# Optimization experiments

Measured on AMD Instinct MI355X. Metric: run time of the kernel, lower is better.

Reference implementation:

```python
import jax, jax.numpy as jnp
import numpy as np

H = 8          # nhead
EPS_Z = 1e-6   # linear-attention normalizer eps
LN_EPS = 1e-5  # torch LayerNorm default


def _ln(x, g, b):
    m = x.mean(-1, keepdims=True)
    v = ((x - m) ** 2).mean(-1, keepdims=True)
    return (x - m) * jax.lax.rsqrt(v + LN_EPS) * g + b


def setup_inputs() -> dict:
    key = jax.random.key(0)
    ks = jax.random.split(key, 8)
    B, S, E, F = 4, 8192, 512, 2048
    s = 0.02
    return {
        "src": jax.random.normal(ks[0], (B, S, E), jnp.float32),
        "Wq": jax.random.normal(ks[1], (E, E), jnp.float32) * s,
        "bq": jnp.zeros((E,), jnp.float32),
        "Wk": jax.random.normal(ks[2], (E, E), jnp.float32) * s,
        "bk": jnp.zeros((E,), jnp.float32),
        "Wv": jax.random.normal(ks[3], (E, E), jnp.float32) * s,
        "bv": jnp.zeros((E,), jnp.float32),
        "Wo": jax.random.normal(ks[4], (E, E), jnp.float32) * s,
        "bo": jnp.zeros((E,), jnp.float32),
        "W1": jax.random.normal(ks[5], (E, F), jnp.float32) * s,
        "b1": jnp.zeros((F,), jnp.float32),
        "W2": jax.random.normal(ks[6], (F, E), jnp.float32) * s,
        "b2": jnp.zeros((E,), jnp.float32),
        "g1": jnp.ones((E,), jnp.float32),
        "be1": jnp.zeros((E,), jnp.float32),
        "g2": jnp.ones((E,), jnp.float32),
        "be2": jnp.zeros((E,), jnp.float32),
    }


def reference(src, Wq, bq, Wk, bk, Wv, bv, Wo, bo, W1, b1, W2, b2, g1, be1, g2, be2):
    B, S, E = src.shape
    Dh = E // H

    def heads(x):  # [B,S,E] -> [B,H,S,Dh]
        return x.reshape(B, S, H, Dh).transpose(0, 2, 1, 3)

    q = heads(src @ Wq + bq)
    k = heads(src @ Wk + bk)
    v = heads(src @ Wv + bv)

    qm = jax.nn.elu(q) + 1.0  # feature map: ELU+1
    km = jax.nn.elu(k) + 1.0

    kv = jnp.einsum("bhsd,bhse->bhde", km, v)          # [B,H,Dh,Dh]
    ksum = km.sum(axis=2)                               # [B,H,Dh]
    z = 1.0 / (jnp.einsum("bhsd,bhd->bhs", qm, ksum) + EPS_Z)
    attn = jnp.einsum("bhsd,bhde->bhse", qm, kv) * z[..., None]

    attn = attn.transpose(0, 2, 1, 3).reshape(B, S, E) @ Wo + bo
    x = _ln(src + attn, g1, be1)
    ff = jax.nn.relu(x @ W1 + b1) @ W2 + b2
    return _ln(x + ff, g2, be2)
```

## Files before the change

kernel.cpp:

```cpp
#include <hip/hip_runtime.h>
#include <hip/hip_bf16.h>

typedef __attribute__((ext_vector_type(8))) short bf16x8;
typedef __attribute__((ext_vector_type(4))) float f32x4;

__device__ inline ushort f2bf(float f) {
    uint u = __float_as_uint(f);
    u += 0x7fff + ((u >> 16) & 1);
    return (ushort)(u >> 16);
}
__device__ inline float bf2f(ushort h) {
    return __uint_as_float(((uint)h) << 16);
}

__device__ inline void gload16(const void* g, void* lds) {
    __builtin_amdgcn_global_load_lds(
        (const __attribute__((address_space(1))) void*)g,
        (__attribute__((address_space(3))) void*)lds, 16, 0, 0);
}

__global__ void conv_bf16(const float* __restrict__ in, ushort* __restrict__ out, int n4) {
    int i = blockIdx.x * 256 + threadIdx.x;
    if (i >= n4) return;
    float4 a = ((const float4*)in)[i];
    ushort4 o;
    o.x = f2bf(a.x); o.y = f2bf(a.y); o.z = f2bf(a.z); o.w = f2bf(a.w);
    ((ushort4*)out)[i] = o;
}

__global__ void wconv_t(const float* __restrict__ in, ushort* __restrict__ out, int K, int N) {
    __shared__ float tile[32][33];
    int kb = blockIdx.y * 32, nb = blockIdx.x * 32;
    int tx = threadIdx.x & 31, ty = threadIdx.x >> 5;
#pragma unroll
    for (int i = 0; i < 4; i++)
        tile[ty + i * 8][tx] = in[(size_t)(kb + ty + i * 8) * N + nb + tx];
    __syncthreads();
#pragma unroll
    for (int i = 0; i < 4; i++) {
        int n = nb + ty + i * 8, k = kb + tx;
        out[(size_t)n * K + k] = f2bf(tile[tx][ty + i * 8]);
    }
}

__global__ void biascat(const float* __restrict__ a, const float* __restrict__ b,
                        const float* __restrict__ c, float* __restrict__ o) {
    int i = blockIdx.x * 256 + threadIdx.x;
    if (i < 512) o[i] = a[i];
    else if (i < 1024) o[i] = b[i - 512];
    else if (i < 1536) o[i] = c[i - 1024];
}

template <int EPI>
__global__ __launch_bounds__(512, 2) void gemm256(
    const ushort* __restrict__ A, const ushort* __restrict__ Bt,
    const float* __restrict__ bias, const ushort* __restrict__ res16,
    ushort* __restrict__ out16, int M, int N, int K, int nbx) {
    extern __shared__ char smem[];
    const int t = threadIdx.x;
    const int w = t >> 6, l = t & 63;
    const int wr = w >> 2, wc = w & 3;
    const int nwg = gridDim.x;
    const int cpx = nwg >> 3;
    const int swz = (blockIdx.x & 7) * cpx + (blockIdx.x >> 3);
    const int bx = swz % nbx, by = swz / nbx;

    const int sc = (t & 3) ^ ((t >> 3) & 3);
    const ushort* gA0 = A + (size_t)(by * 256 + (t >> 2)) * K + sc * 8;
    const ushort* gA1 = gA0 + (size_t)128 * K;
    const ushort* gB0 = Bt + (size_t)(bx * 256 + (t >> 2)) * K + sc * 8;
    const ushort* gB1 = gB0 + (size_t)128 * K;

#define STAGE_H0(kt)                                          \
    {                                                         \
        char* Lb = smem + ((kt) & 3) * 32768 + (w << 10);     \
        const int ko_ = (kt) * 32;                            \
        gload16(gA0 + ko_, Lb);                               \
        gload16(gB0 + ko_, Lb + 16384);                       \
    }
#define STAGE_H1(kt)                                          \
    {                                                         \
        char* Lb = smem + ((kt) & 3) * 32768 + (w << 10);     \
        const int ko_ = (kt) * 32;                            \
        gload16(gA1 + ko_, Lb + 8192);                        \
        gload16(gB1 + ko_, Lb + 24576);                       \
    }

    f32x4 acc[8][4] = {};
    const int Kt = K >> 5;

    const int R0a = wr * 128 + (l & 15);
    const int offA = R0a * 64 + (((l >> 4) ^ ((R0a >> 1) & 3)) << 4);
    const int R0b = wc * 64 + (l & 15);
    const int offB = 16384 + R0b * 64 + (((l >> 4) ^ ((R0b >> 1) & 3)) << 4);

    STAGE_H0(0); STAGE_H1(0);
    STAGE_H0(1); STAGE_H1(1);
    STAGE_H0(2); STAGE_H1(2);

#pragma unroll 1
    for (int kt = 0; kt < Kt; ++kt) {
        const int rem = Kt - 1 - kt;
        if (rem >= 2)      asm volatile("s_waitcnt vmcnt(8)" ::: "memory");
        else if (rem == 1) asm volatile("s_waitcnt vmcnt(4)" ::: "memory");
        else               asm volatile("s_waitcnt vmcnt(0)" ::: "memory");
        __builtin_amdgcn_s_barrier();
        __builtin_amdgcn_sched_barrier(0);

        const char* bufp = smem + (kt & 3) * 32768;
        bf16x8 a[8], b[4];
        b[0] = *(const bf16x8*)(bufp + offB);
        b[1] = *(const bf16x8*)(bufp + offB + 1024);
        b[2] = *(const bf16x8*)(bufp + offB + 2048);
        b[3] = *(const bf16x8*)(bufp + offB + 3072);
        a[0] = *(const bf16x8*)(bufp + offA);
        a[1] = *(const bf16x8*)(bufp + offA + 1024);
        a[2] = *(const bf16x8*)(bufp + offA + 2048);
        a[3] = *(const bf16x8*)(bufp + offA + 3072);
        if (kt + 3 < Kt) STAGE_H0(kt + 3);
        __builtin_amdgcn_sched_barrier(0);
        __builtin_amdgcn_s_barrier();
        asm volatile("s_waitcnt lgkmcnt(0)" ::: "memory");
        __builtin_amdgcn_sched_barrier(0);
        __builtin_amdgcn_s_setprio(1);
#pragma unroll
        for (int m = 0; m < 4; m++)
#pragma unroll
            for (int n = 0; n < 4; n++)
                acc[m][n] = __builtin_amdgcn_mfma_f32_16x16x32_bf16(a[m], b[n], acc[m][n], 0, 0, 0);
        __builtin_amdgcn_s_setprio(0);
        __builtin_amdgcn_sched_barrier(0);
        a[4] = *(const bf16x8*)(bufp + offA + 4096);
        a[5] = *(const bf16x8*)(bufp + offA + 5120);
        a[6] = *(const bf16x8*)(bufp + offA + 6144);
        a[7] = *(const bf16x8*)(bufp + offA + 7168);
        if (kt + 3 < Kt) STAGE_H1(kt + 3);
        __builtin_amdgcn_sched_barrier(0);
        __builtin_amdgcn_s_barrier();
        asm volatile("s_waitcnt lgkmcnt(0)" ::: "memory");
        __builtin_amdgcn_sched_barrier(0);
        __builtin_amdgcn_s_setprio(1);
#pragma unroll
        for (int m = 4; m < 8; m++)
#pragma unroll
            for (int n = 0; n < 4; n++)
                acc[m][n] = __builtin_amdgcn_mfma_f32_16x16x32_bf16(a[m], b[n], acc[m][n], 0, 0, 0);
        __builtin_amdgcn_s_setprio(0);
        __builtin_amdgcn_sched_barrier(0);
    }
#undef STAGE_H0
#undef STAGE_H1

    const int row0 = by * 256 + wr * 128 + ((l >> 4) << 2);
    const int col0 = bx * 256 + wc * 64 + (l & 15);
    const int seg = bx >> 1;
    const size_t segoff = (size_t)seg * M * 512;
    const int c511 = col0 & 511;
    float bv[4];
#pragma unroll
    for (int n = 0; n < 4; n++) bv[n] = bias[col0 + n * 16];
#pragma unroll
    for (int m = 0; m < 8; m++) {
#pragma unroll
        for (int r = 0; r < 4; r++) {
            const int row = row0 + m * 16 + r;
            const size_t base = (size_t)row * N + col0;
#pragma unroll
            for (int n = 0; n < 4; n++) {
                float vv = acc[m][n][r] + bv[n];
                if constexpr (EPI == 2) {
                    vv = vv > 0.f ? vv : 0.f;
                    out16[base + n * 16] = f2bf(vv);
                } else if constexpr (EPI == 3) {
                    vv += bf2f(res16[base + n * 16]);
                    out16[base + n * 16] = f2bf(vv);
                } else if constexpr (EPI == 4) {
                    if (seg < 2) vv = vv > 0.f ? vv + 1.f : __expf(vv);
                    out16[segoff + (size_t)row * 512 + c511 + n * 16] = f2bf(vv);
                } else {
                    out16[base + n * 16] = f2bf(vv);
                }
            }
        }
    }
}

__global__ __launch_bounds__(256) void kv_partial(
    const ushort* __restrict__ km, const ushort* __restrict__ v,
    float* __restrict__ kvp, float* __restrict__ ksump, int S) {
    __shared__ ushort kms[32 * 64];
    __shared__ ushort vs[32 * 64];
    const int t = threadIdx.x;
    const int bh = blockIdx.y, b = bh >> 3, h = bh & 7;
    const int d0 = (t >> 4) * 4, e0 = (t & 15) * 4;
    float acc[4][4] = {};
    float ks = 0.f;
    const int s_base = blockIdx.x * 512;
    const int r = t >> 3, c8 = (t & 7) * 8;
    for (int s0 = 0; s0 < 512; s0 += 32) {
        size_t grow = ((size_t)b * S + s_base + s0 + r) * 512 + h * 64 + c8;
        *(uint4*)&kms[r * 64 + c8] = *(const uint4*)&km[grow];
        *(uint4*)&vs[r * 64 + c8] = *(const uint4*)&v[grow];
        __syncthreads();
#pragma unroll 4
        for (int s = 0; s < 32; ++s) {
            ushort4 ka = *(const ushort4*)&kms[s * 64 + d0];
            ushort4 vb = *(const ushort4*)&vs[s * 64 + e0];
            float a0 = bf2f(ka.x), a1 = bf2f(ka.y), a2 = bf2f(ka.z), a3 = bf2f(ka.w);
            float b0 = bf2f(vb.x), b1 = bf2f(vb.y), b2 = bf2f(vb.z), b3 = bf2f(vb.w);
            acc[0][0] += a0 * b0; acc[0][1] += a0 * b1; acc[0][2] += a0 * b2; acc[0][3] += a0 * b3;
            acc[1][0] += a1 * b0; acc[1][1] += a1 * b1; acc[1][2] += a1 * b2; acc[1][3] += a1 * b3;
            acc[2][0] += a2 * b0; acc[2][1] += a2 * b1; acc[2][2] += a2 * b2; acc[2][3] += a2 * b3;
            acc[3][0] += a3 * b0; acc[3][1] += a3 * b1; acc[3][2] += a3 * b2; acc[3][3] += a3 * b3;
            if (t < 64) ks += bf2f(kms[s * 64 + t]);
        }
        __syncthreads();
    }
    float* dst = kvp + ((size_t)bh * 16 + blockIdx.x) * 4096;
#pragma unroll
    for (int i = 0; i < 4; i++)
#pragma unroll
        for (int j = 0; j < 4; j++)
            dst[(d0 + i) * 64 + e0 + j] = acc[i][j];
    if (t < 64) ksump[((size_t)bh * 16 + blockIdx.x) * 64 + t] = ks;
}

__global__ void kv_reduce(const float* __restrict__ kvp, const float* __restrict__ ksump,
                          ushort* __restrict__ kvt, float* __restrict__ ksum) {
    int i = blockIdx.x * 256 + threadIdx.x;
    if (i < 32 * 4096) {
        int bh = i >> 12, de = i & 4095;
        int d = de >> 6, e = de & 63;
        float s = 0.f;
#pragma unroll
        for (int c = 0; c < 16; ++c) s += kvp[((size_t)bh * 16 + c) * 4096 + de];
        kvt[(size_t)bh * 4096 + e * 64 + d] = f2bf(s);
    } else {
        int j = i - 32 * 4096;
        if (j < 32 * 64) {
            int bh = j >> 6, d = j & 63;
            float s = 0.f;
#pragma unroll
            for (int c = 0; c < 16; ++c) s += ksump[((size_t)bh * 16 + c) * 64 + d];
            ksum[j] = s;
        }
    }
}

__global__ __launch_bounds__(256) void attn_mfma(
    const ushort* __restrict__ qm, const ushort* __restrict__ kvt,
    const float* __restrict__ ksum, ushort* __restrict__ attnE, int S) {
    __shared__ ushort As[128 * 128];
    __shared__ ushort Bs[128 * 64];
    __shared__ float zbuf[128][2];
    __shared__ float ks2[128];
    const int t = threadIdx.x, w = t >> 6, l = t & 63;
    const int cx = blockIdx.x, by = blockIdx.y;
    const int b = (by * 128) / S;
    const int h0 = cx * 2;
    const size_t arow0 = (size_t)(by * 128) * 512 + cx * 128;

#pragma unroll
    for (int rd = 0; rd < 8; ++rd) {
        const ushort* g = qm + arow0 + (size_t)(rd * 16 + w * 4 + (l >> 4)) * 512 + (l & 15) * 8;
        gload16(g, (char*)As + rd * 4096 + w * 1024);
    }
    const ushort* kvbase = kvt + (size_t)(b * 8 + h0) * 4096;
#pragma unroll
    for (int rd = 0; rd < 4; ++rd) {
        const ushort* g = kvbase + (rd * 32 + w * 8 + (l >> 3)) * 64 + (l & 7) * 8;
        gload16(g, (char*)Bs + rd * 4096 + w * 1024);
    }
    if (t < 128) ks2[t] = ksum[(b * 8 + h0) * 64 + t];
    __syncthreads();

    {
        const int r = t >> 1, hh = t & 1;
        float den = 0.f;
#pragma unroll
        for (int d0 = 0; d0 < 64; d0 += 8) {
            bf16x8 qv = *(const bf16x8*)&As[r * 128 + hh * 64 + d0];
#pragma unroll
            for (int j = 0; j < 8; j++) den += bf2f((ushort)qv[j]) * ks2[hh * 64 + d0 + j];
        }
        zbuf[r][hh] = 1.0f / (den + 1e-6f);
    }

    const int wr = w >> 1, wc = w & 1;
    const int ar = wr * 64 + (l & 15);
    const int br = wc * 64 + (l & 15);
    const int ko = (l >> 4) * 8;
    f32x4 acc[4][4] = {};
#pragma unroll
    for (int ks_ = 0; ks_ < 2; ++ks_) {
        bf16x8 a[4], bb[4];
#pragma unroll
        for (int m = 0; m < 4; m++)
            a[m] = *(const bf16x8*)&As[(ar + m * 16) * 128 + wc * 64 + ks_ * 32 + ko];
#pragma unroll
        for (int n = 0; n < 4; n++)
            bb[n] = *(const bf16x8*)&Bs[(br + n * 16) * 64 + ks_ * 32 + ko];
#pragma unroll
        for (int m = 0; m < 4; m++)
#pragma unroll
            for (int n = 0; n < 4; n++)
                acc[m][n] = __builtin_amdgcn_mfma_f32_16x16x32_bf16(a[m], bb[n], acc[m][n], 0, 0, 0);
    }
    __syncthreads();

    const int row0l = wr * 64 + ((l >> 4) << 2);
    ushort* outbase = attnE + (size_t)(by * 128) * 512 + cx * 128;
#pragma unroll
    for (int n = 0; n < 4; n++) {
#pragma unroll
        for (int m = 0; m < 4; m++) {
#pragma unroll
            for (int r = 0; r < 4; r++) {
                int rl = row0l + m * 16 + r;
                float z = zbuf[rl][wc];
                outbase[(size_t)rl * 512 + wc * 64 + n * 16 + (l & 15)] = f2bf(acc[m][n][r] * z);
            }
        }
    }
}

template <int OUT32>
__global__ __launch_bounds__(256) void ln_bf16(
    const ushort* __restrict__ in, const float* __restrict__ g, const float* __restrict__ be,
    void* __restrict__ outp, int Mrows) {
    const int w = threadIdx.x >> 6, l = threadIdx.x & 63;
    const int row = blockIdx.x * 4 + w;
    if (row >= Mrows) return;
    const ushort* rp = in + (size_t)row * 512;
    uint4 u = *(const uint4*)&rp[l * 8];
    float x[8];
    x[0] = bf2f((ushort)(u.x & 0xffff)); x[1] = bf2f((ushort)(u.x >> 16));
    x[2] = bf2f((ushort)(u.y & 0xffff)); x[3] = bf2f((ushort)(u.y >> 16));
    x[4] = bf2f((ushort)(u.z & 0xffff)); x[5] = bf2f((ushort)(u.z >> 16));
    x[6] = bf2f((ushort)(u.w & 0xffff)); x[7] = bf2f((ushort)(u.w >> 16));
    float s = 0.f, ss = 0.f;
#pragma unroll
    for (int j = 0; j < 8; j++) { s += x[j]; ss += x[j] * x[j]; }
#pragma unroll
    for (int o = 1; o < 64; o <<= 1) {
        s += __shfl_xor(s, o, 64);
        ss += __shfl_xor(ss, o, 64);
    }
    float mean = s * (1.f / 512.f);
    float var = ss * (1.f / 512.f) - mean * mean;
    float rstd = rsqrtf(var + 1e-5f);
    float4 g0 = *(const float4*)&g[l * 8], g1v = *(const float4*)&g[l * 8 + 4];
    float4 b0 = *(const float4*)&be[l * 8], b1v = *(const float4*)&be[l * 8 + 4];
    float o0[8];
    o0[0] = (x[0] - mean) * rstd * g0.x + b0.x;
    o0[1] = (x[1] - mean) * rstd * g0.y + b0.y;
    o0[2] = (x[2] - mean) * rstd * g0.z + b0.z;
    o0[3] = (x[3] - mean) * rstd * g0.w + b0.w;
    o0[4] = (x[4] - mean) * rstd * g1v.x + b1v.x;
    o0[5] = (x[5] - mean) * rstd * g1v.y + b1v.y;
    o0[6] = (x[6] - mean) * rstd * g1v.z + b1v.z;
    o0[7] = (x[7] - mean) * rstd * g1v.w + b1v.w;
    if constexpr (OUT32) {
        float* op = (float*)outp + (size_t)row * 512;
        *(float4*)&op[l * 8] = make_float4(o0[0], o0[1], o0[2], o0[3]);
        *(float4*)&op[l * 8 + 4] = make_float4(o0[4], o0[5], o0[6], o0[7]);
    } else {
        ushort* op = (ushort*)outp + (size_t)row * 512;
        ushort4 u0, u1;
        u0.x = f2bf(o0[0]); u0.y = f2bf(o0[1]); u0.z = f2bf(o0[2]); u0.w = f2bf(o0[3]);
        u1.x = f2bf(o0[4]); u1.y = f2bf(o0[5]); u1.z = f2bf(o0[6]); u1.w = f2bf(o0[7]);
        *(ushort4*)&op[l * 8] = u0;
        *(ushort4*)&op[l * 8 + 4] = u1;
    }
}

extern "C" void kernel_launch(void* const* d_in, const int* in_sizes, int n_in,
                              void* d_out, int out_size, void* d_ws, size_t ws_size,
                              hipStream_t stream) {
    const int B = 4, S = 8192, E = 512, F = 2048;
    const int M = B * S;
    const size_t SZ = (size_t)M * E * 2;
    const int SMEM = 131072;

    const float* src = (const float*)d_in[0];
    const float* Wq = (const float*)d_in[1];  const float* bq = (const float*)d_in[2];
    const float* Wk = (const float*)d_in[3];  const float* bk = (const float*)d_in[4];
    const float* Wv = (const float*)d_in[5];  const float* bv = (const float*)d_in[6];
    const float* Wo = (const float*)d_in[7];  const float* bo = (const float*)d_in[8];
    const float* W1 = (const float*)d_in[9];  const float* b1 = (const float*)d_in[10];
    const float* W2 = (const float*)d_in[11]; const float* b2 = (const float*)d_in[12];
    const float* g1 = (const float*)d_in[13]; const float* be1 = (const float*)d_in[14];
    const float* g2 = (const float*)d_in[15]; const float* be2 = (const float*)d_in[16];

    char* ws = (char*)d_ws;
    ushort* qm    = (ushort*)(ws + 0 * SZ);
    ushort* km    = (ushort*)(ws + 1 * SZ);
    ushort* v     = (ushort*)(ws + 2 * SZ);
    ushort* src16 = (ushort*)(ws + 3 * SZ);
    ushort* x16   = (ushort*)(ws + 4 * SZ);
    ushort* z16   = (ushort*)(ws + 5 * SZ);
    char*   tail  = ws + 6 * SZ;
    float*  kvp   = (float*)(tail);
    float*  ksump = (float*)(tail + 8388608);
    ushort* kvt   = (ushort*)(tail + 8519680);
    float*  ksum  = (float*)(tail + 8781824);
    float*  bqkv  = (float*)(tail + 8790016);
    ushort* wqkv  = (ushort*)(tail + 8796160);
    ushort* wot   = (ushort*)(tail + 10369024);
    ushort* w1t   = (ushort*)(tail + 10893312);
    ushort* w2t   = (ushort*)(tail + 12990464);
    ushort* attnE = km;
    ushort* y16   = v;
    ushort* hbuf  = (ushort*)(ws + 0);

    hipFuncSetAttribute((const void*)gemm256<2>, hipFuncAttributeMaxDynamicSharedMemorySize, SMEM);
    hipFuncSetAttribute((const void*)gemm256<3>, hipFuncAttributeMaxDynamicSharedMemorySize, SMEM);
    hipFuncSetAttribute((const void*)gemm256<4>, hipFuncAttributeMaxDynamicSharedMemorySize, SMEM);

    conv_bf16<<<dim3((M * E / 4 + 255) / 256), 256, 0, stream>>>(src, src16, M * E / 4);
    wconv_t<<<dim3(E / 32, E / 32), 256, 0, stream>>>(Wq, wqkv, E, E);
    wconv_t<<<dim3(E / 32, E / 32), 256, 0, stream>>>(Wk, wqkv + 512 * 512, E, E);
    wconv_t<<<dim3(E / 32, E / 32), 256, 0, stream>>>(Wv, wqkv + 1024 * 512, E, E);
    wconv_t<<<dim3(E / 32, E / 32), 256, 0, stream>>>(Wo, wot, E, E);
    wconv_t<<<dim3(F / 32, E / 32), 256, 0, stream>>>(W1, w1t, E, F);
    wconv_t<<<dim3(E / 32, F / 32), 256, 0, stream>>>(W2, w2t, F, E);
    biascat<<<dim3(6), 256, 0, stream>>>(bq, bk, bv, bqkv);

    gemm256<4><<<dim3(6 * 128), 512, SMEM, stream>>>(src16, wqkv, bqkv, nullptr, qm, M, 1536, E, 6);

    kv_partial<<<dim3(16, 32), 256, 0, stream>>>(km, v, kvp, ksump, S);
    kv_reduce<<<dim3((32 * 4096 + 32 * 64 + 255) / 256), 256, 0, stream>>>(kvp, ksump, kvt, ksum);

    attn_mfma<<<dim3(4, M / 128), 256, 0, stream>>>(qm, kvt, ksum, attnE, S);

    gemm256<3><<<dim3(2 * 128), 512, SMEM, stream>>>(attnE, wot, bo, src16, y16, M, E, E, 2);
    ln_bf16<0><<<dim3(M / 4), 256, 0, stream>>>(y16, g1, be1, x16, M);

    gemm256<2><<<dim3(8 * 128), 512, SMEM, stream>>>(x16, w1t, b1, nullptr, hbuf, M, F, E, 8);
    gemm256<3><<<dim3(2 * 128), 512, SMEM, stream>>>(hbuf, w2t, b2, x16, z16, M, E, F, 2);
    ln_bf16<1><<<dim3(M / 4), 256, 0, stream>>>(z16, g2, be2, (float*)d_out, M);
}
```

Baseline: 382.8 us.

## Add 128x128-tile GEMM kernel for QKV, out-proj and FFN1 GEMMs

Adds a new gemm128 kernel with 128x128 tiles, 4 waves, double-buffered 32-wide K stages in 32KB of LDS, and the same fused epilogues. It replaces the 256x256 kernel for the QKV projection, the output projection and the first FFN GEMM, and keeps gemm256 only for the K=2048 FFN2 GEMM. The aim is more workgroups and higher occupancy with less LDS per block for the short-K GEMMs. The cost is lower data reuse per tile and more global loads.

```diff
diff --git a/kernel.cpp b/kernel.cpp
--- a/kernel.cpp
+++ b/kernel.cpp
@@ -161,6 +161,130 @@
     for (int n = 0; n < 4; n++) bv[n] = bias[col0 + n * 16];
 #pragma unroll
     for (int m = 0; m < 8; m++) {
+#pragma unroll
+        for (int r = 0; r < 4; r++) {
+            const int row = row0 + m * 16 + r;
+            const size_t base = (size_t)row * N + col0;
+#pragma unroll
+            for (int n = 0; n < 4; n++) {
+                float vv = acc[m][n][r] + bv[n];
+                if constexpr (EPI == 2) {
+                    vv = vv > 0.f ? vv : 0.f;
+                    out16[base + n * 16] = f2bf(vv);
+                } else if constexpr (EPI == 3) {
+                    vv += bf2f(res16[base + n * 16]);
+                    out16[base + n * 16] = f2bf(vv);
+                } else if constexpr (EPI == 4) {
+                    if (seg < 2) vv = vv > 0.f ? vv + 1.f : __expf(vv);
+                    out16[segoff + (size_t)row * 512 + c511 + n * 16] = f2bf(vv);
+                } else {
+                    out16[base + n * 16] = f2bf(vv);
+                }
+            }
+        }
+    }
+}
+
+template <int EPI>
+__global__ __launch_bounds__(256) void gemm128(
+    const ushort* __restrict__ A, const ushort* __restrict__ Bt,
+    const float* __restrict__ bias, const ushort* __restrict__ res16,
+    ushort* __restrict__ out16, int M, int N, int K, int nbx) {
+    extern __shared__ char smem[];
+    const int t = threadIdx.x;
+    const int w = t >> 6, l = t & 63;
+    const int wr = w >> 1, wc = w & 1;
+    const int nwg = gridDim.x;
+    const int cpx = nwg >> 3;
+    const int swz = (blockIdx.x & 7) * cpx + (blockIdx.x >> 3);
+    const int bx = swz % nbx, by = swz / nbx;
+
+    const int sc = (t & 3) ^ ((t >> 3) & 3);
+    const ushort* gA0 = A + (size_t)(by * 128 + (t >> 2)) * K + sc * 8;
+    const ushort* gA1 = gA0 + (size_t)64 * K;
+    const ushort* gB0 = Bt + (size_t)(bx * 128 + (t >> 2)) * K + sc * 8;
+    const ushort* gB1 = gB0 + (size_t)64 * K;
+
+#define STAGE(kt)                                             \
+    {                                                         \
+        char* Lb = smem + ((kt) & 1) * 16384 + (w << 10);     \
+        const int ko_ = (kt) * 32;                            \
+        gload16(gA0 + ko_, Lb);                               \
+        gload16(gA1 + ko_, Lb + 4096);                        \
+        gload16(gB0 + ko_, Lb + 8192);                        \
+        gload16(gB1 + ko_, Lb + 12288);                       \
+    }
+
+    f32x4 acc[4][4] = {};
+    const int Kt = K >> 5;
+
+    const int R0a = wr * 64 + (l & 15);
+    const int offA = R0a * 64 + (((l >> 4) ^ ((R0a >> 1) & 3)) << 4);
+    const int R0b = wc * 64 + (l & 15);
+    const int offB = 8192 + R0b * 64 + (((l >> 4) ^ ((R0b >> 1) & 3)) << 4);
+
+    STAGE(0);
+
+#pragma unroll 1
+    for (int kt = 0; kt < Kt; ++kt) {
+        if (kt + 1 < Kt) {
+            STAGE(kt + 1);
+            asm volatile("s_waitcnt vmcnt(4)" ::: "memory");
+        } else {
+            asm volatile("s_waitcnt vmcnt(0)" ::: "memory");
+        }
+        __builtin_amdgcn_s_barrier();
+        __builtin_amdgcn_sched_barrier(0);
+
+        const char* bufp = smem + (kt & 1) * 16384;
+        bf16x8 a[4], b[4];
+        b[0] = *(const bf16x8*)(bufp + offB);
+        b[1] = *(const bf16x8*)(bufp + offB + 1024);
+        b[2] = *(const bf16x8*)(bufp + offB + 2048);
+        b[3] = *(const bf16x8*)(bufp + offB + 3072);
+        a[0] = *(const bf16x8*)(bufp + offA);
+        a[1] = *(const bf16x8*)(bufp + offA + 1024);
+        __builtin_amdgcn_sched_barrier(0);
+        __builtin_amdgcn_s_barrier();
+        asm volatile("s_waitcnt lgkmcnt(0)" ::: "memory");
+        __builtin_amdgcn_sched_barrier(0);
+        __builtin_amdgcn_s_setprio(1);
+#pragma unroll
+        for (int m = 0; m < 2; m++)
+#pragma unroll
+            for (int n = 0; n < 4; n++)
+                acc[m][n] = __builtin_amdgcn_mfma_f32_16x16x32_bf16(a[m], b[n], acc[m][n], 0, 0, 0);
+        __builtin_amdgcn_s_setprio(0);
+        __builtin_amdgcn_sched_barrier(0);
+        a[2] = *(const bf16x8*)(bufp + offA + 2048);
+        a[3] = *(const bf16x8*)(bufp + offA + 3072);
+        __builtin_amdgcn_sched_barrier(0);
+        __builtin_amdgcn_s_barrier();
+        asm volatile("s_waitcnt lgkmcnt(0)" ::: "memory");
+        __builtin_amdgcn_sched_barrier(0);
+        __builtin_amdgcn_s_setprio(1);
+#pragma unroll
+        for (int m = 2; m < 4; m++)
+#pragma unroll
+            for (int n = 0; n < 4; n++)
+                acc[m][n] = __builtin_amdgcn_mfma_f32_16x16x32_bf16(a[m], b[n], acc[m][n], 0, 0, 0);
+        __builtin_amdgcn_s_setprio(0);
+        __builtin_amdgcn_sched_barrier(0);
+        __builtin_amdgcn_s_barrier();
+        __builtin_amdgcn_sched_barrier(0);
+    }
+#undef STAGE
+
+    const int row0 = by * 128 + wr * 64 + ((l >> 4) << 2);
+    const int col0 = bx * 128 + wc * 64 + (l & 15);
+    const int seg = bx >> 2;
+    const size_t segoff = (size_t)seg * M * 512;
+    const int c511 = col0 & 511;
+    float bv[4];
+#pragma unroll
+    for (int n = 0; n < 4; n++) bv[n] = bias[col0 + n * 16];
+#pragma unroll
+    for (int m = 0; m < 4; m++) {
 #pragma unroll
         for (int r = 0; r < 4; r++) {
             const int row = row0 + m * 16 + r;
@@ -380,7 +504,8 @@
     const int B = 4, S = 8192, E = 512, F = 2048;
     const int M = B * S;
     const size_t SZ = (size_t)M * E * 2;
-    const int SMEM = 131072;
+    const int SMEM256 = 131072;
+    const int SMEM128 = 32768;
 
     const float* src = (const float*)d_in[0];
     const float* Wq = (const float*)d_in[1];  const float* bq = (const float*)d_in[2];
@@ -413,9 +538,7 @@
     ushort* y16   = v;
     ushort* hbuf  = (ushort*)(ws + 0);
 
-    hipFuncSetAttribute((const void*)gemm256<2>, hipFuncAttributeMaxDynamicSharedMemorySize, SMEM);
-    hipFuncSetAttribute((const void*)gemm256<3>, hipFuncAttributeMaxDynamicSharedMemorySize, SMEM);
-    hipFuncSetAttribute((const void*)gemm256<4>, hipFuncAttributeMaxDynamicSharedMemorySize, SMEM);
+    hipFuncSetAttribute((const void*)gemm256<3>, hipFuncAttributeMaxDynamicSharedMemorySize, SMEM256);
 
     conv_bf16<<<dim3((M * E / 4 + 255) / 256), 256, 0, stream>>>(src, src16, M * E / 4);
     wconv_t<<<dim3(E / 32, E / 32), 256, 0, stream>>>(Wq, wqkv, E, E);
@@ -426,17 +549,17 @@
     wconv_t<<<dim3(E / 32, F / 32), 256, 0, stream>>>(W2, w2t, F, E);
     biascat<<<dim3(6), 256, 0, stream>>>(bq, bk, bv, bqkv);
 
-    gemm256<4><<<dim3(6 * 128), 512, SMEM, stream>>>(src16, wqkv, bqkv, nullptr, qm, M, 1536, E, 6);
+    gemm128<4><<<dim3(12 * 256), 256, SMEM128, stream>>>(src16, wqkv, bqkv, nullptr, qm, M, 1536, E, 12);
 
     kv_partial<<<dim3(16, 32), 256, 0, stream>>>(km, v, kvp, ksump, S);
     kv_reduce<<<dim3((32 * 4096 + 32 * 64 + 255) / 256), 256, 0, stream>>>(kvp, ksump, kvt, ksum);
 
     attn_mfma<<<dim3(4, M / 128), 256, 0, stream>>>(qm, kvt, ksum, attnE, S);
 
-    gemm256<3><<<dim3(2 * 128), 512, SMEM, stream>>>(attnE, wot, bo, src16, y16, M, E, E, 2);
+    gemm128<3><<<dim3(4 * 256), 256, SMEM128, stream>>>(attnE, wot, bo, src16, y16, M, E, E, 4);
     ln_bf16<0><<<dim3(M / 4), 256, 0, stream>>>(y16, g1, be1, x16, M);
 
-    gemm256<2><<<dim3(8 * 128), 512, SMEM, stream>>>(x16, w1t, b1, nullptr, hbuf, M, F, E, 8);
-    gemm256<3><<<dim3(2 * 128), 512, SMEM, stream>>>(hbuf, w2t, b2, x16, z16, M, E, F, 2);
+    gemm128<2><<<dim3(16 * 256), 256, SMEM128, stream>>>(x16, w1t, b1, nullptr, hbuf, M, F, E, 16);
+    gemm256<3><<<dim3(2 * 128), 512, SMEM256, stream>>>(hbuf, w2t, b2, x16, z16, M, E, F, 2);
     ln_bf16<1><<<dim3(M / 4), 256, 0, stream>>>(z16, g2, be2, (float*)d_out, M);
 }
```

New measurement: 393.7 us. +2.8%, slower.

## Make GEMM blocks persistent over multiple N tiles with continuous prefetch pipeline

Applied to the files above, without the earlier changes.

The GEMM kernel gains a template parameter NT so each workgroup computes NT consecutive 256-wide column tiles for the same row block. The global-to-LDS prefetch pipeline runs across tile boundaries, so there is no refill bubble between tiles. The QKV and FFN1 GEMMs now launch 256 blocks instead of 768/1024, which removes tail effects and repeated prologues. In exchange, parallelism drops to one wave of blocks and the A tile is reloaded for each N tile.

```diff
diff --git a/kernel.cpp b/kernel.cpp
--- a/kernel.cpp
+++ b/kernel.cpp
@@ -51,11 +51,11 @@
     else if (i < 1536) o[i] = c[i - 1024];
 }
 
-template <int EPI>
+template <int EPI, int NT>
 __global__ __launch_bounds__(512, 2) void gemm256(
     const ushort* __restrict__ A, const ushort* __restrict__ Bt,
     const float* __restrict__ bias, const ushort* __restrict__ res16,
-    ushort* __restrict__ out16, int M, int N, int K, int nbx) {
+    ushort* __restrict__ out16, int M, int N, int K, int nbxg) {
     extern __shared__ char smem[];
     const int t = threadIdx.x;
     const int w = t >> 6, l = t & 63;
@@ -63,123 +63,140 @@
     const int nwg = gridDim.x;
     const int cpx = nwg >> 3;
     const int swz = (blockIdx.x & 7) * cpx + (blockIdx.x >> 3);
-    const int bx = swz % nbx, by = swz / nbx;
+    const int bxg = swz % nbxg, by = swz / nbxg;
+    const int bx0 = bxg * NT;
 
     const int sc = (t & 3) ^ ((t >> 3) & 3);
     const ushort* gA0 = A + (size_t)(by * 256 + (t >> 2)) * K + sc * 8;
     const ushort* gA1 = gA0 + (size_t)128 * K;
-    const ushort* gB0 = Bt + (size_t)(bx * 256 + (t >> 2)) * K + sc * 8;
-    const ushort* gB1 = gB0 + (size_t)128 * K;
-
-#define STAGE_H0(kt)                                          \
-    {                                                         \
-        char* Lb = smem + ((kt) & 3) * 32768 + (w << 10);     \
-        const int ko_ = (kt) * 32;                            \
-        gload16(gA0 + ko_, Lb);                               \
-        gload16(gB0 + ko_, Lb + 16384);                       \
-    }
-#define STAGE_H1(kt)                                          \
-    {                                                         \
-        char* Lb = smem + ((kt) & 3) * 32768 + (w << 10);     \
-        const int ko_ = (kt) * 32;                            \
-        gload16(gA1 + ko_, Lb + 8192);                        \
-        gload16(gB1 + ko_, Lb + 24576);                       \
-    }
+    const ushort* sB0 = Bt + (size_t)(bx0 * 256 + (t >> 2)) * K + sc * 8;
+    const ushort* sB1 = sB0 + (size_t)128 * K;
+
+    const int Kt = K >> 5;
+    const int TOT = NT * Kt;
+    int stg_kt = 0, stg_g = 0;
+
+    auto stage_h0 = [&]() {
+        char* Lb = smem + (stg_g & 3) * 32768 + (w << 10);
+        gload16(gA0 + stg_kt * 32, Lb);
+        gload16(sB0 + stg_kt * 32, Lb + 16384);
+    };
+    auto stage_h1 = [&]() {
+        char* Lb = smem + (stg_g & 3) * 32768 + (w << 10);
+        gload16(gA1 + stg_kt * 32, Lb + 8192);
+        gload16(sB1 + stg_kt * 32, Lb + 24576);
+        ++stg_g;
+        if (++stg_kt == Kt) {
+            stg_kt = 0;
+            sB0 += (size_t)256 * K;
+            sB1 += (size_t)256 * K;
+        }
+    };
 
     f32x4 acc[8][4] = {};
-    const int Kt = K >> 5;
 
     const int R0a = wr * 128 + (l & 15);
     const int offA = R0a * 64 + (((l >> 4) ^ ((R0a >> 1) & 3)) << 4);
     const int R0b = wc * 64 + (l & 15);
     const int offB = 16384 + R0b * 64 + (((l >> 4) ^ ((R0b >> 1) & 3)) << 4);
 
-    STAGE_H0(0); STAGE_H1(0);
-    STAGE_H0(1); STAGE_H1(1);
-    STAGE_H0(2); STAGE_H1(2);
-
+    stage_h0(); stage_h1();
+    stage_h0(); stage_h1();
+    stage_h0(); stage_h1();
+
+    int g = 0;
+    for (int j = 0; j < NT; ++j) {
 #pragma unroll 1
-    for (int kt = 0; kt < Kt; ++kt) {
-        const int rem = Kt - 1 - kt;
-        if (rem >= 2)      asm volatile("s_waitcnt vmcnt(8)" ::: "memory");
-        else if (rem == 1) asm volatile("s_waitcnt vmcnt(4)" ::: "memory");
-        else               asm volatile("s_waitcnt vmcnt(0)" ::: "memory");
-        __builtin_amdgcn_s_barrier();
-        __builtin_amdgcn_sched_barrier(0);
-
-        const char* bufp = smem + (kt & 3) * 32768;
-        bf16x8 a[8], b[4];
-        b[0] = *(const bf16x8*)(bufp + offB);
-        b[1] = *(const bf16x8*)(bufp + offB + 1024);
-        b[2] = *(const bf16x8*)(bufp + offB + 2048);
-        b[3] = *(const bf16x8*)(bufp + offB + 3072);
-        a[0] = *(const bf16x8*)(bufp + offA);
-        a[1] = *(const bf16x8*)(bufp + offA + 1024);
-        a[2] = *(const bf16x8*)(bufp + offA + 2048);
-        a[3] = *(const bf16x8*)(bufp + offA + 3072);
-        if (kt + 3 < Kt) STAGE_H0(kt + 3);
-        __builtin_amdgcn_sched_barrier(0);
-        __builtin_amdgcn_s_barrier();
-        asm volatile("s_waitcnt lgkmcnt(0)" ::: "memory");
-        __builtin_amdgcn_sched_barrier(0);
-        __builtin_amdgcn_s_setprio(1);
-#pragma unroll
-        for (int m = 0; m < 4; m++)
-#pragma unroll
-            for (int n = 0; n < 4; n++)
-                acc[m][n] = __builtin_amdgcn_mfma_f32_16x16x32_bf16(a[m], b[n], acc[m][n], 0, 0, 0);
-        __builtin_amdgcn_s_setprio(0);
-        __builtin_amdgcn_sched_barrier(0);
-        a[4] = *(const bf16x8*)(bufp + offA + 4096);
-        a[5] = *(const bf16x8*)(bufp + offA + 5120);
-        a[6] = *(const bf16x8*)(bufp + offA + 6144);
-        a[7] = *(const bf16x8*)(bufp + offA + 7168);
-        if (kt + 3 < Kt) STAGE_H1(kt + 3);
-        __builtin_amdgcn_sched_barrier(0);
-        __builtin_amdgcn_s_barrier();
-        asm volatile("s_waitcnt lgkmcnt(0)" ::: "memory");
-        __builtin_amdgcn_sched_barrier(0);
-        __builtin_amdgcn_s_setprio(1);
-#pragma unroll
-        for (int m = 4; m < 8; m++)
-#pragma unroll
-            for (int n = 0; n < 4; n++)
-                acc[m][n] = __builtin_amdgcn_mfma_f32_16x16x32_bf16(a[m], b[n], acc[m][n], 0, 0, 0);
-        __builtin_amdgcn_s_setprio(0);
-        __builtin_amdgcn_sched_barrier(0);
-    }
-#undef STAGE_H0
-#undef STAGE_H1
-
-    const int row0 = by * 256 + wr * 128 + ((l >> 4) << 2);
-    const int col0 = bx * 256 + wc * 64 + (l & 15);
-    const int seg = bx >> 1;
-    const size_t segoff = (size_t)seg * M * 512;
-    const int c511 = col0 & 511;
-    float bv[4];
-#pragma unroll
-    for (int n = 0; n < 4; n++) bv[n] = bias[col0 + n * 16];
-#pragma unroll
-    for (int m = 0; m < 8; m++) {
-#pragma unroll
-        for (int r = 0; r < 4; r++) {
-            const int row = row0 + m * 16 + r;
-            const size_t base = (size_t)row * N + col0;
-#pragma unroll
-            for (int n = 0; n < 4; n++) {
-                float vv = acc[m][n][r] + bv[n];
-                if constexpr (EPI == 2) {
-                    vv = vv > 0.f ? vv : 0.f;
-                    out16[base + n * 16] = f2bf(vv);
-                } else if constexpr (EPI == 3) {
-                    vv += bf2f(res16[base + n * 16]);
-                    out16[base + n * 16] = f2bf(vv);
-                } else if constexpr (EPI == 4) {
-                    if (seg < 2) vv = vv > 0.f ? vv + 1.f : __expf(vv);
-                    out16[segoff + (size_t)row * 512 + c511 + n * 16] = f2bf(vv);
-                } else {
-                    out16[base + n * 16] = f2bf(vv);
+        for (int kt = 0; kt < Kt; ++kt, ++g) {
+            const int rem = TOT - 1 - g;
+            if (rem >= 2)      asm volatile("s_waitcnt vmcnt(8)" ::: "memory");
+            else if (rem == 1) asm volatile("s_waitcnt vmcnt(4)" ::: "memory");
+            else               asm volatile("s_waitcnt vmcnt(0)" ::: "memory");
+            __builtin_amdgcn_s_barrier();
+            __builtin_amdgcn_sched_barrier(0);
+
+            const char* bufp = smem + (g & 3) * 32768;
+            bf16x8 a[8], b[4];
+            b[0] = *(const bf16x8*)(bufp + offB);
+            b[1] = *(const bf16x8*)(bufp + offB + 1024);
+            b[2] = *(const bf16x8*)(bufp + offB + 2048);
+            b[3] = *(const bf16x8*)(bufp + offB + 3072);
+            a[0] = *(const bf16x8*)(bufp + offA);
+            a[1] = *(const bf16x8*)(bufp + offA + 1024);
+            a[2] = *(const bf16x8*)(bufp + offA + 2048);
+            a[3] = *(const bf16x8*)(bufp + offA + 3072);
+            if (g + 3 < TOT) stage_h0();
+            __builtin_amdgcn_sched_barrier(0);
+            __builtin_amdgcn_s_barrier();
+            asm volatile("s_waitcnt lgkmcnt(0)" ::: "memory");
+            __builtin_amdgcn_sched_barrier(0);
+            __builtin_amdgcn_s_setprio(1);
+#pragma unroll
+            for (int m = 0; m < 4; m++)
+#pragma unroll
+                for (int n = 0; n < 4; n++)
+                    acc[m][n] = __builtin_amdgcn_mfma_f32_16x16x32_bf16(a[m], b[n], acc[m][n], 0, 0, 0);
+            __builtin_amdgcn_s_setprio(0);
+            __builtin_amdgcn_sched_barrier(0);
+            a[4] = *(const bf16x8*)(bufp + offA + 4096);
+            a[5] = *(const bf16x8*)(bufp + offA + 5120);
+            a[6] = *(const bf16x8*)(bufp + offA + 6144);
+            a[7] = *(const bf16x8*)(bufp + offA + 7168);
+            if (g + 3 < TOT) stage_h1();
+            __builtin_amdgcn_sched_barrier(0);
+            __builtin_amdgcn_s_barrier();
+            asm volatile("s_waitcnt lgkmcnt(0)" ::: "memory");
+            __builtin_amdgcn_sched_barrier(0);
+            __builtin_amdgcn_s_setprio(1);
+#pragma unroll
+            for (int m = 4; m < 8; m++)
+#pragma unroll
+                for (int n = 0; n < 4; n++)
+                    acc[m][n] = __builtin_amdgcn_mfma_f32_16x16x32_bf16(a[m], b[n], acc[m][n], 0, 0, 0);
+            __builtin_amdgcn_s_setprio(0);
+            __builtin_amdgcn_sched_barrier(0);
+        }
+
+        {
+            const int bx = bx0 + j;
+            const int row0 = by * 256 + wr * 128 + ((l >> 4) << 2);
+            const int col0 = bx * 256 + wc * 64 + (l & 15);
+            const int seg = bx >> 1;
+            const size_t segoff = (size_t)seg * M * 512;
+            const int c511 = col0 & 511;
+            float bv[4];
+#pragma unroll
+            for (int n = 0; n < 4; n++) bv[n] = bias[col0 + n * 16];
+#pragma unroll
+            for (int m = 0; m < 8; m++) {
+#pragma unroll
+                for (int r = 0; r < 4; r++) {
+                    const int row = row0 + m * 16 + r;
+                    const size_t base = (size_t)row * N + col0;
+#pragma unroll
+                    for (int n = 0; n < 4; n++) {
+                        float vv = acc[m][n][r] + bv[n];
+                        if constexpr (EPI == 2) {
+                            vv = vv > 0.f ? vv : 0.f;
+                            out16[base + n * 16] = f2bf(vv);
+                        } else if constexpr (EPI == 3) {
+                            vv += bf2f(res16[base + n * 16]);
+                            out16[base + n * 16] = f2bf(vv);
+                        } else if constexpr (EPI == 4) {
+                            if (seg < 2) vv = vv > 0.f ? vv + 1.f : __expf(vv);
+                            out16[segoff + (size_t)row * 512 + c511 + n * 16] = f2bf(vv);
+                        } else {
+                            out16[base + n * 16] = f2bf(vv);
+                        }
+                    }
                 }
+            }
+            if (j + 1 < NT) {
+#pragma unroll
+                for (int m = 0; m < 8; m++)
+#pragma unroll
+                    for (int n = 0; n < 4; n++)
+                        acc[m][n] = (f32x4){0.f, 0.f, 0.f, 0.f};
             }
         }
     }
@@ -413,9 +430,9 @@
     ushort* y16   = v;
     ushort* hbuf  = (ushort*)(ws + 0);
 
-    hipFuncSetAttribute((const void*)gemm256<2>, hipFuncAttributeMaxDynamicSharedMemorySize, SMEM);
-    hipFuncSetAttribute((const void*)gemm256<3>, hipFuncAttributeMaxDynamicSharedMemorySize, SMEM);
-    hipFuncSetAttribute((const void*)gemm256<4>, hipFuncAttributeMaxDynamicSharedMemorySize, SMEM);
+    hipFuncSetAttribute((const void*)gemm256<4, 3>, hipFuncAttributeMaxDynamicSharedMemorySize, SMEM);
+    hipFuncSetAttribute((const void*)gemm256<3, 1>, hipFuncAttributeMaxDynamicSharedMemorySize, SMEM);
+    hipFuncSetAttribute((const void*)gemm256<2, 4>, hipFuncAttributeMaxDynamicSharedMemorySize, SMEM);
 
     conv_bf16<<<dim3((M * E / 4 + 255) / 256), 256, 0, stream>>>(src, src16, M * E / 4);
     wconv_t<<<dim3(E / 32, E / 32), 256, 0, stream>>>(Wq, wqkv, E, E);
@@ -426,17 +443,17 @@
     wconv_t<<<dim3(E / 32, F / 32), 256, 0, stream>>>(W2, w2t, F, E);
     biascat<<<dim3(6), 256, 0, stream>>>(bq, bk, bv, bqkv);
 
-    gemm256<4><<<dim3(6 * 128), 512, SMEM, stream>>>(src16, wqkv, bqkv, nullptr, qm, M, 1536, E, 6);
+    gemm256<4, 3><<<dim3(2 * 128), 512, SMEM, stream>>>(src16, wqkv, bqkv, nullptr, qm, M, 1536, E, 2);
 
     kv_partial<<<dim3(16, 32), 256, 0, stream>>>(km, v, kvp, ksump, S);
     kv_reduce<<<dim3((32 * 4096 + 32 * 64 + 255) / 256), 256, 0, stream>>>(kvp, ksump, kvt, ksum);
 
     attn_mfma<<<dim3(4, M / 128), 256, 0, stream>>>(qm, kvt, ksum, attnE, S);
 
-    gemm256<3><<<dim3(2 * 128), 512, SMEM, stream>>>(attnE, wot, bo, src16, y16, M, E, E, 2);
+    gemm256<3, 1><<<dim3(2 * 128), 512, SMEM, stream>>>(attnE, wot, bo, src16, y16, M, E, E, 2);
     ln_bf16<0><<<dim3(M / 4), 256, 0, stream>>>(y16, g1, be1, x16, M);
 
-    gemm256<2><<<dim3(8 * 128), 512, SMEM, stream>>>(x16, w1t, b1, nullptr, hbuf, M, F, E, 8);
-    gemm256<3><<<dim3(2 * 128), 512, SMEM, stream>>>(hbuf, w2t, b2, x16, z16, M, E, F, 2);
+    gemm256<2, 4><<<dim3(2 * 128), 512, SMEM, stream>>>(x16, w1t, b1, nullptr, hbuf, M, F, E, 2);
+    gemm256<3, 1><<<dim3(2 * 128), 512, SMEM, stream>>>(hbuf, w2t, b2, x16, z16, M, E, F, 2);
     ln_bf16<1><<<dim3(M / 4), 256, 0, stream>>>(z16, g2, be2, (float*)d_out, M);
 }
```

New measurement: 379.4 us. Within noise of the previous version (-0.9%).
